# Kernel optimization log

Hardware: AMD Instinct MI355X
Metric: run time of the kernel (lower is better)

## Reference

```python
import jax, jax.numpy as jnp
import numpy as np

D_MODEL = 1024
NUM_HEADS = 16
HEAD_DIM = D_MODEL // NUM_HEADS

def setup_inputs() -> dict:
    key = jax.random.key(0)
    ks = jax.random.split(key, 9)
    B, L = 2, 2048
    s = 1.0 / np.sqrt(D_MODEL)
    return {
        "x":  jax.random.normal(ks[0], (B, L, D_MODEL), dtype=jnp.float32),
        "Wq": jax.random.uniform(ks[1], (D_MODEL, D_MODEL), jnp.float32, -s, s),
        "bq": jax.random.uniform(ks[2], (D_MODEL,), jnp.float32, -s, s),
        "Wk": jax.random.uniform(ks[3], (D_MODEL, D_MODEL), jnp.float32, -s, s),
        "bk": jax.random.uniform(ks[4], (D_MODEL,), jnp.float32, -s, s),
        "Wv": jax.random.uniform(ks[5], (D_MODEL, D_MODEL), jnp.float32, -s, s),
        "bv": jax.random.uniform(ks[6], (D_MODEL,), jnp.float32, -s, s),
        "Wo": jax.random.uniform(ks[7], (D_MODEL, D_MODEL), jnp.float32, -s, s),
        "bo": jax.random.uniform(ks[8], (D_MODEL,), jnp.float32, -s, s),
    }

def _split_heads(t):
    B, L, _ = t.shape
    return t.reshape(B, L, NUM_HEADS, HEAD_DIM).transpose(0, 2, 1, 3)  # [B,H,L,Dh]

def reference(x, Wq, bq, Wk, bk, Wv, bv, Wo, bo):
    # Linear projections (torch Linear: y = x @ W.T + b)
    Q = _split_heads(x @ Wq.T + bq)
    K = _split_heads(x @ Wk.T + bk)
    V = _split_heads(x @ Wv.T + bv)
    scale = 1.0 / jnp.sqrt(jnp.asarray(HEAD_DIM, dtype=x.dtype))
    scores = jnp.einsum('bhqd,bhkd->bhqk', Q, K) * scale  # [B,H,L,L]
    attn_weights = jax.nn.softmax(scores, axis=-1)
    ctx = jnp.einsum('bhqk,bhkd->bhqd', attn_weights, V)  # [B,H,L,Dh]
    B, H, L, Dh = ctx.shape
    ctx = ctx.transpose(0, 2, 1, 3).reshape(B, L, H * Dh)
    out = ctx @ Wo.T + bo  # dropout p=0.0 -> identity
    return (out, attn_weights)
```

## Files before the change

### kernel.cpp

```cpp
#include <hip/hip_runtime.h>

typedef unsigned short u16;
typedef __bf16 bf16x8 __attribute__((ext_vector_type(8)));
typedef float f32x4 __attribute__((ext_vector_type(4)));

#define LSTR 40
#define WSTR 72

__device__ __forceinline__ u16 f2bf(float f) {
    union { float f; unsigned int u; } v; v.f = f;
    unsigned int u = v.u;
    u += 0x7fffu + ((u >> 16) & 1u);
    return (u16)(u >> 16);
}

__device__ __forceinline__ u16 cvt_bf(float f) {
    __bf16 h = (__bf16)f;
    union { __bf16 h; u16 u; } v; v.h = h; return v.u;
}

__device__ __forceinline__ void stage8_bf(const u16* __restrict__ g, u16* __restrict__ lds) {
    *(uint4*)lds = *(const uint4*)g;
}

__device__ __forceinline__ void gload16(const u16* g, u16* l) {
    __builtin_amdgcn_global_load_lds((const __attribute__((address_space(1))) unsigned int*)(const void*)g,
                                     (__attribute__((address_space(3))) unsigned int*)(void*)l, 16, 0, 0);
}

__device__ __forceinline__ void mfma_tile(const u16* lA, const u16* lB,
                                          int wm, int wn, int quad, int m16,
                                          f32x4 (&acc)[2][2]) {
    bf16x8 a0 = *(const bf16x8*)(lA + (wm + m16) * LSTR + quad * 8);
    bf16x8 a1 = *(const bf16x8*)(lA + (wm + 16 + m16) * LSTR + quad * 8);
    bf16x8 b0 = *(const bf16x8*)(lB + (wn + m16) * LSTR + quad * 8);
    bf16x8 b1 = *(const bf16x8*)(lB + (wn + 16 + m16) * LSTR + quad * 8);
    acc[0][0] = __builtin_amdgcn_mfma_f32_16x16x32_bf16(a0, b0, acc[0][0], 0, 0, 0);
    acc[0][1] = __builtin_amdgcn_mfma_f32_16x16x32_bf16(a0, b1, acc[0][1], 0, 0, 0);
    acc[1][0] = __builtin_amdgcn_mfma_f32_16x16x32_bf16(a1, b0, acc[1][0], 0, 0, 0);
    acc[1][1] = __builtin_amdgcn_mfma_f32_16x16x32_bf16(a1, b1, acc[1][1], 0, 0, 0);
}

__global__ __launch_bounds__(256) void k_cvtX(const float* __restrict__ src, u16* __restrict__ dst) {
    const size_t i = ((size_t)blockIdx.x * 256 + threadIdx.x) * 8;
    float4 v0 = *(const float4*)(src + i);
    float4 v1 = *(const float4*)(src + i + 4);
    u16 o[8];
    o[0] = f2bf(v0.x); o[1] = f2bf(v0.y); o[2] = f2bf(v0.z); o[3] = f2bf(v0.w);
    o[4] = f2bf(v1.x); o[5] = f2bf(v1.y); o[6] = f2bf(v1.z); o[7] = f2bf(v1.w);
    *(uint4*)(dst + i) = *(const uint4*)o;
}

__global__ __launch_bounds__(256) void k_cvtW(const float* __restrict__ w0, const float* __restrict__ w1,
                                              const float* __restrict__ w2, const float* __restrict__ w3,
                                              u16* __restrict__ dst) {
    const int z = blockIdx.z;
    const float* src = z == 0 ? w0 : z == 1 ? w1 : z == 2 ? w2 : w3;
    const size_t i = ((size_t)blockIdx.x * 256 + threadIdx.x) * 8;
    float4 v0 = *(const float4*)(src + i);
    float4 v1 = *(const float4*)(src + i + 4);
    u16 o[8];
    o[0] = f2bf(v0.x); o[1] = f2bf(v0.y); o[2] = f2bf(v0.z); o[3] = f2bf(v0.w);
    o[4] = f2bf(v1.x); o[5] = f2bf(v1.y); o[6] = f2bf(v1.z); o[7] = f2bf(v1.w);
    *(uint4*)(dst + (size_t)z * 1048576 + i) = *(const uint4*)o;
}

__global__ __launch_bounds__(256) void k_qkv(const u16* __restrict__ Xb, const u16* __restrict__ Wb,
                                             const float* __restrict__ bq, const float* __restrict__ bk,
                                             const float* __restrict__ bv,
                                             u16* __restrict__ Q, u16* __restrict__ Kd, u16* __restrict__ Vt) {
    __shared__ __align__(16) u16 lA[128 * 32];
    __shared__ __align__(16) u16 lB[128 * 32];
    const int t = threadIdx.x;
    const int n0 = blockIdx.x * 128;
    const int m0 = blockIdx.y * 128;
    const int lane = t & 63, wave = t >> 6;
    const int wm = (wave >> 1) * 64, wn = (wave & 1) * 64;
    const int quad = lane >> 4, m16 = lane & 15;
    const int r4 = t >> 2, c8 = (t & 3) * 8;
    f32x4 acc[4][4] = {};
    for (int k0 = 0; k0 < 1024; k0 += 32) {
        gload16(Xb + (size_t)(m0 + r4) * 1024 + k0 + c8,       &lA[t * 8]);
        gload16(Xb + (size_t)(m0 + 64 + r4) * 1024 + k0 + c8,  &lA[2048 + t * 8]);
        gload16(Wb + (size_t)(n0 + r4) * 1024 + k0 + c8,       &lB[t * 8]);
        gload16(Wb + (size_t)(n0 + 64 + r4) * 1024 + k0 + c8,  &lB[2048 + t * 8]);
        __syncthreads();
        bf16x8 af[4], bfr[4];
#pragma unroll
        for (int i = 0; i < 4; ++i) {
            af[i]  = *(const bf16x8*)(lA + (wm + i * 16 + m16) * 32 + quad * 8);
            bfr[i] = *(const bf16x8*)(lB + (wn + i * 16 + m16) * 32 + quad * 8);
        }
#pragma unroll
        for (int mi = 0; mi < 4; ++mi)
#pragma unroll
            for (int ni = 0; ni < 4; ++ni)
                acc[mi][ni] = __builtin_amdgcn_mfma_f32_16x16x32_bf16(af[mi], bfr[ni], acc[mi][ni], 0, 0, 0);
        __syncthreads();
    }
#pragma unroll
    for (int ni = 0; ni < 4; ++ni) {
        const int gcol = n0 + wn + ni * 16 + m16;
        const int mat = gcol >> 10;
        const int col = gcol & 1023;
        const int h = col >> 6, d = col & 63;
        const float bias = (mat == 0 ? bq : mat == 1 ? bk : bv)[col];
        u16* dst = mat == 0 ? Q : mat == 1 ? Kd : Vt;
#pragma unroll
        for (int mi = 0; mi < 4; ++mi)
#pragma unroll
            for (int e = 0; e < 4; ++e) {
                const int row = m0 + wm + mi * 16 + quad * 4 + e;
                const int b = row >> 11, l = row & 2047;
                const float v = acc[mi][ni][e] + bias;
                size_t idx;
                if (mat == 2) idx = (((size_t)(b * 16 + h)) * 64 + d) * 2048 + l;
                else          idx = (((size_t)(b * 16 + h)) * 2048 + l) * 64 + d;
                dst[idx] = cvt_bf(v);
            }
    }
}

__global__ __launch_bounds__(256) void k_attn(const u16* __restrict__ Q,
                                              const u16* __restrict__ K,
                                              const u16* __restrict__ Vt,
                                              float* __restrict__ attn,
                                              u16* __restrict__ ctx) {
    __shared__ __align__(16) u16 lK[64 * WSTR];
    __shared__ __align__(16) u16 lV[64 * WSTR];
    __shared__ __align__(16) u16 lW[64 * WSTR];
    __shared__ float sred[2][64];
    const int t = threadIdx.x;
    const int bh = blockIdx.y;
    const int m0 = blockIdx.x * 64;
    const int lane = t & 63, wave = t >> 6;
    const int wq = (wave & 1) * 32;
    const int wk = (wave >> 1) * 32;
    const int wm = (wave >> 1) * 32, wn = (wave & 1) * 32;
    const int quad = lane >> 4, m16 = lane & 15;
    const int sr = t >> 3, sc = (t & 7) * 8;
    const u16* Qh = Q + (size_t)bh * 2048 * 64;
    const u16* Kh = K + (size_t)bh * 2048 * 64;
    const u16* Vh = Vt + (size_t)bh * 64 * 2048;
    float* ah = attn + ((size_t)bh << 22) + (size_t)m0 * 2048;

    const float SC = 0.18033688011112042f;

    bf16x8 qf[2][2];
#pragma unroll
    for (int ni = 0; ni < 2; ++ni)
#pragma unroll
        for (int ks = 0; ks < 2; ++ks)
            qf[ni][ks] = *(const bf16x8*)(Qh + (size_t)(m0 + wq + ni * 16 + m16) * 64 + ks * 32 + quad * 8);

    float slane[2] = {0.f, 0.f};
    {
        const u16* kp = Kh + (size_t)sr * 64 + sc;
        for (int kt = 0; kt < 32; ++kt) {
            __syncthreads();
            *(uint4*)&lK[sr * WSTR + sc]        = *(const uint4*)kp;
            *(uint4*)&lK[(sr + 32) * WSTR + sc] = *(const uint4*)(kp + 32 * 64);
            kp += 64 * 64;
            __syncthreads();
            f32x4 sacc[2][2] = {};
#pragma unroll
            for (int ks = 0; ks < 2; ++ks) {
                bf16x8 a0 = *(const bf16x8*)(lK + (wk + m16) * WSTR + ks * 32 + quad * 8);
                bf16x8 a1 = *(const bf16x8*)(lK + (wk + 16 + m16) * WSTR + ks * 32 + quad * 8);
                sacc[0][0] = __builtin_amdgcn_mfma_f32_16x16x32_bf16(a0, qf[0][ks], sacc[0][0], 0, 0, 0);
                sacc[0][1] = __builtin_amdgcn_mfma_f32_16x16x32_bf16(a0, qf[1][ks], sacc[0][1], 0, 0, 0);
                sacc[1][0] = __builtin_amdgcn_mfma_f32_16x16x32_bf16(a1, qf[0][ks], sacc[1][0], 0, 0, 0);
                sacc[1][1] = __builtin_amdgcn_mfma_f32_16x16x32_bf16(a1, qf[1][ks], sacc[1][1], 0, 0, 0);
            }
#pragma unroll
            for (int mi = 0; mi < 2; ++mi)
#pragma unroll
                for (int e = 0; e < 4; ++e) {
                    slane[0] += __builtin_amdgcn_exp2f(sacc[mi][0][e] * SC);
                    slane[1] += __builtin_amdgcn_exp2f(sacc[mi][1][e] * SC);
                }
        }
    }
#pragma unroll
    for (int ni = 0; ni < 2; ++ni) {
        slane[ni] += __shfl_xor(slane[ni], 16);
        slane[ni] += __shfl_xor(slane[ni], 32);
    }
    if (quad == 0) {
        sred[wave >> 1][wq + m16]      = slane[0];
        sred[wave >> 1][wq + 16 + m16] = slane[1];
    }
    __syncthreads();
    float inv[2];
    inv[0] = 1.0f / (sred[0][wq + m16]      + sred[1][wq + m16]);
    inv[1] = 1.0f / (sred[0][wq + 16 + m16] + sred[1][wq + 16 + m16]);

    unsigned aoff[2][2], lwoff[2][2];
#pragma unroll
    for (int mi = 0; mi < 2; ++mi)
#pragma unroll
        for (int ni = 0; ni < 2; ++ni) {
            const int q = wq + ni * 16 + m16;
            const int k = wk + mi * 16 + quad * 4;
            aoff[mi][ni]  = (unsigned)(q * 2048 + k);
            lwoff[mi][ni] = (unsigned)(q * WSTR + k);
        }

    f32x4 cacc[2][2] = {};
    {
        const u16* kp = Kh + (size_t)sr * 64 + sc;
        const u16* vp = Vh + (size_t)sr * 2048 + sc;
        for (int kt = 0; kt < 32; ++kt) {
            __syncthreads();
            *(uint4*)&lK[sr * WSTR + sc]        = *(const uint4*)kp;
            *(uint4*)&lK[(sr + 32) * WSTR + sc] = *(const uint4*)(kp + 32 * 64);
            *(uint4*)&lV[sr * WSTR + sc]        = *(const uint4*)vp;
            *(uint4*)&lV[(sr + 32) * WSTR + sc] = *(const uint4*)(vp + 32 * 2048);
            kp += 64 * 64; vp += 64;
            __syncthreads();
            f32x4 sacc[2][2] = {};
#pragma unroll
            for (int ks = 0; ks < 2; ++ks) {
                bf16x8 a0 = *(const bf16x8*)(lK + (wk + m16) * WSTR + ks * 32 + quad * 8);
                bf16x8 a1 = *(const bf16x8*)(lK + (wk + 16 + m16) * WSTR + ks * 32 + quad * 8);
                sacc[0][0] = __builtin_amdgcn_mfma_f32_16x16x32_bf16(a0, qf[0][ks], sacc[0][0], 0, 0, 0);
                sacc[0][1] = __builtin_amdgcn_mfma_f32_16x16x32_bf16(a0, qf[1][ks], sacc[0][1], 0, 0, 0);
                sacc[1][0] = __builtin_amdgcn_mfma_f32_16x16x32_bf16(a1, qf[0][ks], sacc[1][0], 0, 0, 0);
                sacc[1][1] = __builtin_amdgcn_mfma_f32_16x16x32_bf16(a1, qf[1][ks], sacc[1][1], 0, 0, 0);
            }
#pragma unroll
            for (int mi = 0; mi < 2; ++mi)
#pragma unroll
                for (int ni = 0; ni < 2; ++ni) {
#pragma unroll
                    for (int e = 0; e < 4; ++e)
                        sacc[mi][ni][e] = __builtin_amdgcn_exp2f(sacc[mi][ni][e] * SC) * inv[ni];
                    u16 p[4];
                    p[0] = cvt_bf(sacc[mi][ni][0]); p[1] = cvt_bf(sacc[mi][ni][1]);
                    p[2] = cvt_bf(sacc[mi][ni][2]); p[3] = cvt_bf(sacc[mi][ni][3]);
                    *(uint2*)&lW[lwoff[mi][ni]] = *(const uint2*)p;
                }
            __syncthreads();
            float* ap = ah + kt * 64;
#pragma unroll
            for (int mi = 0; mi < 2; ++mi)
#pragma unroll
                for (int ni = 0; ni < 2; ++ni)
                    *(f32x4*)(ap + aoff[mi][ni]) = sacc[mi][ni];
#pragma unroll
            for (int ks = 0; ks < 2; ++ks) {
                bf16x8 a0 = *(const bf16x8*)(lW + (wm + m16) * WSTR + ks * 32 + quad * 8);
                bf16x8 a1 = *(const bf16x8*)(lW + (wm + 16 + m16) * WSTR + ks * 32 + quad * 8);
                bf16x8 b0 = *(const bf16x8*)(lV + (wn + m16) * WSTR + ks * 32 + quad * 8);
                bf16x8 b1 = *(const bf16x8*)(lV + (wn + 16 + m16) * WSTR + ks * 32 + quad * 8);
                cacc[0][0] = __builtin_amdgcn_mfma_f32_16x16x32_bf16(a0, b0, cacc[0][0], 0, 0, 0);
                cacc[0][1] = __builtin_amdgcn_mfma_f32_16x16x32_bf16(a0, b1, cacc[0][1], 0, 0, 0);
                cacc[1][0] = __builtin_amdgcn_mfma_f32_16x16x32_bf16(a1, b0, cacc[1][0], 0, 0, 0);
                cacc[1][1] = __builtin_amdgcn_mfma_f32_16x16x32_bf16(a1, b1, cacc[1][1], 0, 0, 0);
            }
        }
    }

#pragma unroll
    for (int mi = 0; mi < 2; ++mi)
#pragma unroll
        for (int ni = 0; ni < 2; ++ni)
#pragma unroll
            for (int e = 0; e < 4; ++e) {
                const int row = m0 + wm + mi * 16 + quad * 4 + e;
                const int col = wn + ni * 16 + m16;
                ctx[(size_t)bh * 2048 * 64 + (size_t)row * 64 + col] = cvt_bf(cacc[mi][ni][e]);
            }
}

__global__ __launch_bounds__(256) void k_out(const u16* __restrict__ ctx,
                                             const u16* __restrict__ WoB,
                                             const float* __restrict__ bo,
                                             float* __restrict__ out) {
    __shared__ __align__(16) u16 lA[64 * LSTR];
    __shared__ __align__(16) u16 lB[64 * LSTR];
    const int t = threadIdx.x;
    const int n0 = blockIdx.x * 64, m0 = blockIdx.y * 64;
    const int lane = t & 63, wave = t >> 6;
    const int wm = (wave >> 1) * 32, wn = (wave & 1) * 32;
    const int quad = lane >> 4, m16 = lane & 15;
    const int r = t >> 2, c8 = (t & 3) * 8;
    const int m = m0 + r;
    const int b = m >> 11, l = m & 2047;
    f32x4 acc[2][2] = {};
    for (int k0 = 0; k0 < 1024; k0 += 32) {
        const int kk = k0 + c8;
        const int h = kk >> 6, d = kk & 63;
        stage8_bf(ctx + (((size_t)(b * 16 + h) * 2048 + l) * 64 + d), &lA[r * LSTR + c8]);
        stage8_bf(WoB + (size_t)(n0 + r) * 1024 + k0 + c8, &lB[r * LSTR + c8]);
        __syncthreads();
        mfma_tile(lA, lB, wm, wn, quad, m16, acc);
        __syncthreads();
    }
#pragma unroll
    for (int mi = 0; mi < 2; ++mi)
#pragma unroll
        for (int ni = 0; ni < 2; ++ni) {
            const int col = n0 + wn + ni * 16 + m16;
            const float bv = bo[col];
#pragma unroll
            for (int e = 0; e < 4; ++e) {
                const int row = m0 + wm + mi * 16 + quad * 4 + e;
                out[(size_t)row * 1024 + col] = acc[mi][ni][e] + bv;
            }
        }
}

extern "C" void kernel_launch(void* const* d_in, const int* in_sizes, int n_in,
                              void* d_out, int out_size, void* d_ws, size_t ws_size,
                              hipStream_t stream) {
    const float* x  = (const float*)d_in[0];
    const float* Wq = (const float*)d_in[1];
    const float* bq = (const float*)d_in[2];
    const float* Wk = (const float*)d_in[3];
    const float* bk = (const float*)d_in[4];
    const float* Wv = (const float*)d_in[5];
    const float* bv = (const float*)d_in[6];
    const float* Wo = (const float*)d_in[7];
    const float* bo = (const float*)d_in[8];

    float* out_f = (float*)d_out;
    float* attn  = out_f + (size_t)4096 * 1024;

    u16* Xb = (u16*)d_ws;
    u16* Wb = Xb + (size_t)4194304;
    u16* Qb = Wb + (size_t)4194304;
    u16* Kb = Qb + (size_t)4194304;
    u16* Vt = Kb + (size_t)4194304;

    dim3 blk(256);
    k_cvtX<<<dim3(2048), blk, 0, stream>>>(x, Xb);
    k_cvtW<<<dim3(512, 1, 4), blk, 0, stream>>>(Wq, Wk, Wv, Wo, Wb);
    k_qkv<<<dim3(24, 32), blk, 0, stream>>>(Xb, Wb, bq, bk, bv, Qb, Kb, Vt);
    k_attn<<<dim3(32, 32), blk, 0, stream>>>(Qb, Kb, Vt, attn, Qb);
    k_out<<<dim3(16, 64), blk, 0, stream>>>(Qb, Wb + (size_t)3072 * 1024, bo, out_f);
}
```

Baseline: 780.2 us.

## Load K/V fragments directly into registers, double-buffer P, retile output GEMM

The attention kernel now loads K and V MFMA fragments straight from global memory into registers and prefetches the next K tile, instead of staging through LDS with two barriers per iteration. The P tile uses a double-buffered LDS slot so only one barrier per step remains. Context is written in [B,L,H*Dh] layout into the X workspace, which lets the output projection use contiguous rows. That GEMM moves to 128x128 tiles with global_load_lds and 4x4 MFMA per wave. Risks are uncoalesced direct fragment loads, higher register pressure, and bank conflicts on the unpadded stride-32 LDS layout.

```diff
diff --git a/kernel.cpp b/kernel.cpp
--- a/kernel.cpp
+++ b/kernel.cpp
@@ -4,7 +4,6 @@
 typedef __bf16 bf16x8 __attribute__((ext_vector_type(8)));
 typedef float f32x4 __attribute__((ext_vector_type(4)));
 
-#define LSTR 40
 #define WSTR 72
 
 __device__ __forceinline__ u16 f2bf(float f) {
@@ -19,26 +18,9 @@
     union { __bf16 h; u16 u; } v; v.h = h; return v.u;
 }
 
-__device__ __forceinline__ void stage8_bf(const u16* __restrict__ g, u16* __restrict__ lds) {
-    *(uint4*)lds = *(const uint4*)g;
-}
-
 __device__ __forceinline__ void gload16(const u16* g, u16* l) {
     __builtin_amdgcn_global_load_lds((const __attribute__((address_space(1))) unsigned int*)(const void*)g,
                                      (__attribute__((address_space(3))) unsigned int*)(void*)l, 16, 0, 0);
-}
-
-__device__ __forceinline__ void mfma_tile(const u16* lA, const u16* lB,
-                                          int wm, int wn, int quad, int m16,
-                                          f32x4 (&acc)[2][2]) {
-    bf16x8 a0 = *(const bf16x8*)(lA + (wm + m16) * LSTR + quad * 8);
-    bf16x8 a1 = *(const bf16x8*)(lA + (wm + 16 + m16) * LSTR + quad * 8);
-    bf16x8 b0 = *(const bf16x8*)(lB + (wn + m16) * LSTR + quad * 8);
-    bf16x8 b1 = *(const bf16x8*)(lB + (wn + 16 + m16) * LSTR + quad * 8);
-    acc[0][0] = __builtin_amdgcn_mfma_f32_16x16x32_bf16(a0, b0, acc[0][0], 0, 0, 0);
-    acc[0][1] = __builtin_amdgcn_mfma_f32_16x16x32_bf16(a0, b1, acc[0][1], 0, 0, 0);
-    acc[1][0] = __builtin_amdgcn_mfma_f32_16x16x32_bf16(a1, b0, acc[1][0], 0, 0, 0);
-    acc[1][1] = __builtin_amdgcn_mfma_f32_16x16x32_bf16(a1, b1, acc[1][1], 0, 0, 0);
 }
 
 __global__ __launch_bounds__(256) void k_cvtX(const float* __restrict__ src, u16* __restrict__ dst) {
@@ -121,14 +103,14 @@
     }
 }
 
+#define MFMA16(A, B, C) __builtin_amdgcn_mfma_f32_16x16x32_bf16(A, B, C, 0, 0, 0)
+
 __global__ __launch_bounds__(256) void k_attn(const u16* __restrict__ Q,
                                               const u16* __restrict__ K,
                                               const u16* __restrict__ Vt,
                                               float* __restrict__ attn,
                                               u16* __restrict__ ctx) {
-    __shared__ __align__(16) u16 lK[64 * WSTR];
-    __shared__ __align__(16) u16 lV[64 * WSTR];
-    __shared__ __align__(16) u16 lW[64 * WSTR];
+    __shared__ __align__(16) u16 lW[2 * 64 * WSTR];
     __shared__ float sred[2][64];
     const int t = threadIdx.x;
     const int bh = blockIdx.y;
@@ -138,7 +120,6 @@
     const int wk = (wave >> 1) * 32;
     const int wm = (wave >> 1) * 32, wn = (wave & 1) * 32;
     const int quad = lane >> 4, m16 = lane & 15;
-    const int sr = t >> 3, sc = (t & 7) * 8;
     const u16* Qh = Q + (size_t)bh * 2048 * 64;
     const u16* Kh = K + (size_t)bh * 2048 * 64;
     const u16* Vh = Vt + (size_t)bh * 64 * 2048;
@@ -153,25 +134,30 @@
         for (int ks = 0; ks < 2; ++ks)
             qf[ni][ks] = *(const bf16x8*)(Qh + (size_t)(m0 + wq + ni * 16 + m16) * 64 + ks * 32 + quad * 8);
 
+    const u16* kpl = Kh + (size_t)(wk + m16) * 64 + quad * 8;
+    const u16* vpl = Vh + (size_t)(wn + m16) * 2048 + quad * 8;
+
     float slane[2] = {0.f, 0.f};
     {
-        const u16* kp = Kh + (size_t)sr * 64 + sc;
+        bf16x8 k00 = *(const bf16x8*)(kpl);
+        bf16x8 k01 = *(const bf16x8*)(kpl + 32);
+        bf16x8 k10 = *(const bf16x8*)(kpl + 1024);
+        bf16x8 k11 = *(const bf16x8*)(kpl + 1024 + 32);
         for (int kt = 0; kt < 32; ++kt) {
-            __syncthreads();
-            *(uint4*)&lK[sr * WSTR + sc]        = *(const uint4*)kp;
-            *(uint4*)&lK[(sr + 32) * WSTR + sc] = *(const uint4*)(kp + 32 * 64);
-            kp += 64 * 64;
-            __syncthreads();
+            const u16* nx = kpl + (size_t)(kt + 1) * 4096;
+            bf16x8 n00 = *(const bf16x8*)(nx);
+            bf16x8 n01 = *(const bf16x8*)(nx + 32);
+            bf16x8 n10 = *(const bf16x8*)(nx + 1024);
+            bf16x8 n11 = *(const bf16x8*)(nx + 1024 + 32);
             f32x4 sacc[2][2] = {};
-#pragma unroll
-            for (int ks = 0; ks < 2; ++ks) {
-                bf16x8 a0 = *(const bf16x8*)(lK + (wk + m16) * WSTR + ks * 32 + quad * 8);
-                bf16x8 a1 = *(const bf16x8*)(lK + (wk + 16 + m16) * WSTR + ks * 32 + quad * 8);
-                sacc[0][0] = __builtin_amdgcn_mfma_f32_16x16x32_bf16(a0, qf[0][ks], sacc[0][0], 0, 0, 0);
-                sacc[0][1] = __builtin_amdgcn_mfma_f32_16x16x32_bf16(a0, qf[1][ks], sacc[0][1], 0, 0, 0);
-                sacc[1][0] = __builtin_amdgcn_mfma_f32_16x16x32_bf16(a1, qf[0][ks], sacc[1][0], 0, 0, 0);
-                sacc[1][1] = __builtin_amdgcn_mfma_f32_16x16x32_bf16(a1, qf[1][ks], sacc[1][1], 0, 0, 0);
-            }
+            sacc[0][0] = MFMA16(k00, qf[0][0], sacc[0][0]);
+            sacc[0][1] = MFMA16(k00, qf[1][0], sacc[0][1]);
+            sacc[1][0] = MFMA16(k10, qf[0][0], sacc[1][0]);
+            sacc[1][1] = MFMA16(k10, qf[1][0], sacc[1][1]);
+            sacc[0][0] = MFMA16(k01, qf[0][1], sacc[0][0]);
+            sacc[0][1] = MFMA16(k01, qf[1][1], sacc[0][1]);
+            sacc[1][0] = MFMA16(k11, qf[0][1], sacc[1][0]);
+            sacc[1][1] = MFMA16(k11, qf[1][1], sacc[1][1]);
 #pragma unroll
             for (int mi = 0; mi < 2; ++mi)
 #pragma unroll
@@ -179,6 +165,7 @@
                     slane[0] += __builtin_amdgcn_exp2f(sacc[mi][0][e] * SC);
                     slane[1] += __builtin_amdgcn_exp2f(sacc[mi][1][e] * SC);
                 }
+            k00 = n00; k01 = n01; k10 = n10; k11 = n11;
         }
     }
 #pragma unroll
@@ -208,37 +195,46 @@
 
     f32x4 cacc[2][2] = {};
     {
-        const u16* kp = Kh + (size_t)sr * 64 + sc;
-        const u16* vp = Vh + (size_t)sr * 2048 + sc;
+        bf16x8 k00 = *(const bf16x8*)(kpl);
+        bf16x8 k01 = *(const bf16x8*)(kpl + 32);
+        bf16x8 k10 = *(const bf16x8*)(kpl + 1024);
+        bf16x8 k11 = *(const bf16x8*)(kpl + 1024 + 32);
+        int buf = 0;
         for (int kt = 0; kt < 32; ++kt) {
-            __syncthreads();
-            *(uint4*)&lK[sr * WSTR + sc]        = *(const uint4*)kp;
-            *(uint4*)&lK[(sr + 32) * WSTR + sc] = *(const uint4*)(kp + 32 * 64);
-            *(uint4*)&lV[sr * WSTR + sc]        = *(const uint4*)vp;
-            *(uint4*)&lV[(sr + 32) * WSTR + sc] = *(const uint4*)(vp + 32 * 2048);
-            kp += 64 * 64; vp += 64;
-            __syncthreads();
+            const u16* nx = kpl + (size_t)(kt + 1) * 4096;
+            bf16x8 n00 = *(const bf16x8*)(nx);
+            bf16x8 n01 = *(const bf16x8*)(nx + 32);
+            bf16x8 n10 = *(const bf16x8*)(nx + 1024);
+            bf16x8 n11 = *(const bf16x8*)(nx + 1024 + 32);
             f32x4 sacc[2][2] = {};
-#pragma unroll
-            for (int ks = 0; ks < 2; ++ks) {
-                bf16x8 a0 = *(const bf16x8*)(lK + (wk + m16) * WSTR + ks * 32 + quad * 8);
-                bf16x8 a1 = *(const bf16x8*)(lK + (wk + 16 + m16) * WSTR + ks * 32 + quad * 8);
-                sacc[0][0] = __builtin_amdgcn_mfma_f32_16x16x32_bf16(a0, qf[0][ks], sacc[0][0], 0, 0, 0);
-                sacc[0][1] = __builtin_amdgcn_mfma_f32_16x16x32_bf16(a0, qf[1][ks], sacc[0][1], 0, 0, 0);
-                sacc[1][0] = __builtin_amdgcn_mfma_f32_16x16x32_bf16(a1, qf[0][ks], sacc[1][0], 0, 0, 0);
-                sacc[1][1] = __builtin_amdgcn_mfma_f32_16x16x32_bf16(a1, qf[1][ks], sacc[1][1], 0, 0, 0);
-            }
+            sacc[0][0] = MFMA16(k00, qf[0][0], sacc[0][0]);
+            sacc[0][1] = MFMA16(k00, qf[1][0], sacc[0][1]);
+            sacc[1][0] = MFMA16(k10, qf[0][0], sacc[1][0]);
+            sacc[1][1] = MFMA16(k10, qf[1][0], sacc[1][1]);
+            sacc[0][0] = MFMA16(k01, qf[0][1], sacc[0][0]);
+            sacc[0][1] = MFMA16(k01, qf[1][1], sacc[0][1]);
+            sacc[1][0] = MFMA16(k11, qf[0][1], sacc[1][0]);
+            sacc[1][1] = MFMA16(k11, qf[1][1], sacc[1][1]);
 #pragma unroll
             for (int mi = 0; mi < 2; ++mi)
 #pragma unroll
-                for (int ni = 0; ni < 2; ++ni) {
+                for (int ni = 0; ni < 2; ++ni)
 #pragma unroll
                     for (int e = 0; e < 4; ++e)
                         sacc[mi][ni][e] = __builtin_amdgcn_exp2f(sacc[mi][ni][e] * SC) * inv[ni];
+            bf16x8 v00 = *(const bf16x8*)(vpl + kt * 64);
+            bf16x8 v01 = *(const bf16x8*)(vpl + kt * 64 + 32);
+            bf16x8 v10 = *(const bf16x8*)(vpl + 32768 + kt * 64);
+            bf16x8 v11 = *(const bf16x8*)(vpl + 32768 + kt * 64 + 32);
+            u16* lwb = lW + buf * (64 * WSTR);
+#pragma unroll
+            for (int mi = 0; mi < 2; ++mi)
+#pragma unroll
+                for (int ni = 0; ni < 2; ++ni) {
                     u16 p[4];
                     p[0] = cvt_bf(sacc[mi][ni][0]); p[1] = cvt_bf(sacc[mi][ni][1]);
                     p[2] = cvt_bf(sacc[mi][ni][2]); p[3] = cvt_bf(sacc[mi][ni][3]);
-                    *(uint2*)&lW[lwoff[mi][ni]] = *(const uint2*)p;
+                    *(uint2*)&lwb[lwoff[mi][ni]] = *(const uint2*)p;
                 }
             __syncthreads();
             float* ap = ah + kt * 64;
@@ -247,20 +243,25 @@
 #pragma unroll
                 for (int ni = 0; ni < 2; ++ni)
                     *(f32x4*)(ap + aoff[mi][ni]) = sacc[mi][ni];
-#pragma unroll
-            for (int ks = 0; ks < 2; ++ks) {
-                bf16x8 a0 = *(const bf16x8*)(lW + (wm + m16) * WSTR + ks * 32 + quad * 8);
-                bf16x8 a1 = *(const bf16x8*)(lW + (wm + 16 + m16) * WSTR + ks * 32 + quad * 8);
-                bf16x8 b0 = *(const bf16x8*)(lV + (wn + m16) * WSTR + ks * 32 + quad * 8);
-                bf16x8 b1 = *(const bf16x8*)(lV + (wn + 16 + m16) * WSTR + ks * 32 + quad * 8);
-                cacc[0][0] = __builtin_amdgcn_mfma_f32_16x16x32_bf16(a0, b0, cacc[0][0], 0, 0, 0);
-                cacc[0][1] = __builtin_amdgcn_mfma_f32_16x16x32_bf16(a0, b1, cacc[0][1], 0, 0, 0);
-                cacc[1][0] = __builtin_amdgcn_mfma_f32_16x16x32_bf16(a1, b0, cacc[1][0], 0, 0, 0);
-                cacc[1][1] = __builtin_amdgcn_mfma_f32_16x16x32_bf16(a1, b1, cacc[1][1], 0, 0, 0);
-            }
-        }
-    }
-
+            bf16x8 a00 = *(const bf16x8*)(lwb + (wm + m16) * WSTR + quad * 8);
+            bf16x8 a01 = *(const bf16x8*)(lwb + (wm + m16) * WSTR + 32 + quad * 8);
+            bf16x8 a10 = *(const bf16x8*)(lwb + (wm + 16 + m16) * WSTR + quad * 8);
+            bf16x8 a11 = *(const bf16x8*)(lwb + (wm + 16 + m16) * WSTR + 32 + quad * 8);
+            cacc[0][0] = MFMA16(a00, v00, cacc[0][0]);
+            cacc[0][1] = MFMA16(a00, v10, cacc[0][1]);
+            cacc[1][0] = MFMA16(a10, v00, cacc[1][0]);
+            cacc[1][1] = MFMA16(a10, v10, cacc[1][1]);
+            cacc[0][0] = MFMA16(a01, v01, cacc[0][0]);
+            cacc[0][1] = MFMA16(a01, v11, cacc[0][1]);
+            cacc[1][0] = MFMA16(a11, v01, cacc[1][0]);
+            cacc[1][1] = MFMA16(a11, v11, cacc[1][1]);
+            k00 = n00; k01 = n01; k10 = n10; k11 = n11;
+            buf ^= 1;
+        }
+    }
+
+    const int b = bh >> 4, h = bh & 15;
+    u16* cp = ctx + ((size_t)b * 2048) * 1024 + h * 64;
 #pragma unroll
     for (int mi = 0; mi < 2; ++mi)
 #pragma unroll
@@ -269,7 +270,7 @@
             for (int e = 0; e < 4; ++e) {
                 const int row = m0 + wm + mi * 16 + quad * 4 + e;
                 const int col = wn + ni * 16 + m16;
-                ctx[(size_t)bh * 2048 * 64 + (size_t)row * 64 + col] = cvt_bf(cacc[mi][ni][e]);
+                cp[(size_t)row * 1024 + col] = cvt_bf(cacc[mi][ni][e]);
             }
 }
 
@@ -277,38 +278,47 @@
                                              const u16* __restrict__ WoB,
                                              const float* __restrict__ bo,
                                              float* __restrict__ out) {
-    __shared__ __align__(16) u16 lA[64 * LSTR];
-    __shared__ __align__(16) u16 lB[64 * LSTR];
+    __shared__ __align__(16) u16 lA[128 * 32];
+    __shared__ __align__(16) u16 lB[128 * 32];
     const int t = threadIdx.x;
-    const int n0 = blockIdx.x * 64, m0 = blockIdx.y * 64;
+    const int n0 = blockIdx.x * 128;
+    const int m0 = blockIdx.y * 128;
     const int lane = t & 63, wave = t >> 6;
-    const int wm = (wave >> 1) * 32, wn = (wave & 1) * 32;
+    const int wm = (wave >> 1) * 64, wn = (wave & 1) * 64;
     const int quad = lane >> 4, m16 = lane & 15;
-    const int r = t >> 2, c8 = (t & 3) * 8;
-    const int m = m0 + r;
-    const int b = m >> 11, l = m & 2047;
-    f32x4 acc[2][2] = {};
+    const int r4 = t >> 2, c8 = (t & 3) * 8;
+    f32x4 acc[4][4] = {};
     for (int k0 = 0; k0 < 1024; k0 += 32) {
-        const int kk = k0 + c8;
-        const int h = kk >> 6, d = kk & 63;
-        stage8_bf(ctx + (((size_t)(b * 16 + h) * 2048 + l) * 64 + d), &lA[r * LSTR + c8]);
-        stage8_bf(WoB + (size_t)(n0 + r) * 1024 + k0 + c8, &lB[r * LSTR + c8]);
+        gload16(ctx + (size_t)(m0 + r4) * 1024 + k0 + c8,       &lA[t * 8]);
+        gload16(ctx + (size_t)(m0 + 64 + r4) * 1024 + k0 + c8,  &lA[2048 + t * 8]);
+        gload16(WoB + (size_t)(n0 + r4) * 1024 + k0 + c8,       &lB[t * 8]);
+        gload16(WoB + (size_t)(n0 + 64 + r4) * 1024 + k0 + c8,  &lB[2048 + t * 8]);
         __syncthreads();
-        mfma_tile(lA, lB, wm, wn, quad, m16, acc);
+        bf16x8 af[4], bfr[4];
+#pragma unroll
+        for (int i = 0; i < 4; ++i) {
+            af[i]  = *(const bf16x8*)(lA + (wm + i * 16 + m16) * 32 + quad * 8);
+            bfr[i] = *(const bf16x8*)(lB + (wn + i * 16 + m16) * 32 + quad * 8);
+        }
+#pragma unroll
+        for (int mi = 0; mi < 4; ++mi)
+#pragma unroll
+            for (int ni = 0; ni < 4; ++ni)
+                acc[mi][ni] = __builtin_amdgcn_mfma_f32_16x16x32_bf16(af[mi], bfr[ni], acc[mi][ni], 0, 0, 0);
         __syncthreads();
     }
 #pragma unroll
-    for (int mi = 0; mi < 2; ++mi)
-#pragma unroll
-        for (int ni = 0; ni < 2; ++ni) {
-            const int col = n0 + wn + ni * 16 + m16;
-            const float bv = bo[col];
+    for (int ni = 0; ni < 4; ++ni) {
+        const int col = n0 + wn + ni * 16 + m16;
+        const float bv = bo[col];
+#pragma unroll
+        for (int mi = 0; mi < 4; ++mi)
 #pragma unroll
             for (int e = 0; e < 4; ++e) {
                 const int row = m0 + wm + mi * 16 + quad * 4 + e;
                 out[(size_t)row * 1024 + col] = acc[mi][ni][e] + bv;
             }
-        }
+    }
 }
 
 extern "C" void kernel_launch(void* const* d_in, const int* in_sizes, int n_in,
@@ -337,6 +347,6 @@
     k_cvtX<<<dim3(2048), blk, 0, stream>>>(x, Xb);
     k_cvtW<<<dim3(512, 1, 4), blk, 0, stream>>>(Wq, Wk, Wv, Wo, Wb);
     k_qkv<<<dim3(24, 32), blk, 0, stream>>>(Xb, Wb, bq, bk, bv, Qb, Kb, Vt);
-    k_attn<<<dim3(32, 32), blk, 0, stream>>>(Qb, Kb, Vt, attn, Qb);
-    k_out<<<dim3(16, 64), blk, 0, stream>>>(Qb, Wb + (size_t)3072 * 1024, bo, out_f);
-}
+    k_attn<<<dim3(32, 32), blk, 0, stream>>>(Qb, Kb, Vt, attn, Xb);
+    k_out<<<dim3(8, 32), blk, 0, stream>>>(Xb, Wb + (size_t)3072 * 1024, bo, out_f);
+}
```

Measured after the change: 845.4 us. 8.3% more time.
